# Performance work log

Hardware: AMD Instinct MI355X
Metric: run time of the kernel (lower is better)

## Reference

```python
import jax, jax.numpy as jnp
import numpy as np
from jax import lax

B, N, C = 8, 4096, 512
NH, R = 8, 8
HD = C // NH
EPS = 1e-3  # keras LayerNormalization default epsilon


def setup_inputs() -> dict:
    key = jax.random.key(0)
    ks = jax.random.split(key, 8)
    s = 0.02
    x = jax.random.normal(ks[0], (B, N, C), dtype=jnp.float32)
    Wq = jax.random.normal(ks[1], (C, C), dtype=jnp.float32) * s
    Wkv = jax.random.normal(ks[2], (C, 2 * C), dtype=jnp.float32) * s
    conv_w = jax.random.normal(ks[3], (R, R, C, C), dtype=jnp.float32) * s  # HWIO
    gamma = jnp.ones((C,), dtype=jnp.float32)
    beta = jnp.zeros((C,), dtype=jnp.float32)
    Wp = jax.random.normal(ks[4], (C, C), dtype=jnp.float32) * s
    bp = jnp.zeros((C,), dtype=jnp.float32)
    return {"x": x, "Wq": Wq, "Wkv": Wkv, "conv_w": conv_w,
            "gamma": gamma, "beta": beta, "Wp": Wp, "bp": bp}


def reference(x, Wq, Wkv, conv_w, gamma, beta, Wp, bp):
    b, n, c = x.shape
    h = w = int(np.sqrt(n))
    scale = 1.0 / np.sqrt(float(HD))

    # queries: Rearrange 'b n (hd nh) -> b n nh hd' then 'b n nh hd -> b nh n hd'
    q = x @ Wq                                   # [B, N, C]
    q = q.reshape(b, n, HD, NH).transpose(0, 3, 1, 2)  # [B, NH, N, HD]

    # spatial reduction of K/V: strided conv (SAME) + layernorm
    fmap = x.reshape(b, h, w, c)
    fmap = lax.conv_general_dilated(
        fmap, conv_w, window_strides=(R, R), padding="SAME",
        dimension_numbers=("NHWC", "HWIO", "NHWC"))   # [B, h/R, w/R, C]
    m = fmap.shape[1] * fmap.shape[2]
    fmap = fmap.reshape(b, m, c)
    mu = jnp.mean(fmap, axis=-1, keepdims=True)
    var = jnp.var(fmap, axis=-1, keepdims=True)
    fmap = (fmap - mu) * lax.rsqrt(var + EPS) * gamma + beta

    # key/value: Rearrange 'b m (f nh hd) -> b m f nh hd', perm [2,0,3,1,4]
    kv = fmap @ Wkv                              # [B, M, 2C]
    kv = kv.reshape(b, m, 2, NH, HD).transpose(2, 0, 3, 1, 4)  # [2, B, NH, M, HD]
    k, v = kv[0], kv[1]

    attn = jax.nn.softmax(jnp.einsum("bhnd,bhmd->bhnm", q, k) * scale, axis=-1)
    out = jnp.einsum("bhnm,bhmd->bhnd", attn, v)  # [B, NH, N, HD]
    out = out.transpose(0, 2, 1, 3).reshape(b, n, c)  # 'b n h c -> b n (h c)'
    return out @ Wp + bp
```

## Files before the change

### kernel.cpp

```cpp
#include <hip/hip_runtime.h>

typedef unsigned short u16;
typedef __bf16 bf16x8 __attribute__((ext_vector_type(8)));
typedef float floatx4 __attribute__((ext_vector_type(4)));

__device__ __forceinline__ u16 f2bf(float f) {
    unsigned u = __float_as_uint(f);
    u += 0x7fff + ((u >> 16) & 1);
    return (u16)(u >> 16);
}

#define GLOAD_LDS16(g, l) __builtin_amdgcn_global_load_lds( \
    (const __attribute__((address_space(1))) void*)(g),      \
    (__attribute__((address_space(3))) void*)(l), 16, 0, 0)

__global__ void cast_f32_bf16(const float* __restrict__ in, u16* __restrict__ out) {
    size_t o = ((size_t)blockIdx.x * 256 + threadIdx.x) * 4;
    float4 v = *(const float4*)(in + o);
    unsigned w0 = (unsigned)f2bf(v.x) | ((unsigned)f2bf(v.y) << 16);
    unsigned w1 = (unsigned)f2bf(v.z) | ((unsigned)f2bf(v.w) << 16);
    *(uint2*)(out + o) = make_uint2(w0, w1);
}

__global__ void transpose_cast(const float* __restrict__ in, u16* __restrict__ out,
                               int R, int Cn) {
    __shared__ float tile[32][33];
    int c0 = blockIdx.x * 32, r0 = blockIdx.y * 32;
    int tx = threadIdx.x, ty = threadIdx.y;
    #pragma unroll
    for (int yy = 0; yy < 4; ++yy)
        tile[ty + yy * 8][tx] = in[(size_t)(r0 + ty + yy * 8) * Cn + c0 + tx];
    __syncthreads();
    #pragma unroll
    for (int yy = 0; yy < 4; ++yy)
        out[(size_t)(c0 + ty + yy * 8) * R + r0 + tx] = f2bf(tile[tx][ty + yy * 8]);
}

__global__ void transpose_cast_qperm(const float* __restrict__ in, u16* __restrict__ out) {
    __shared__ float tile[32][33];
    int c0 = blockIdx.x * 32, r0 = blockIdx.y * 32;
    int tx = threadIdx.x, ty = threadIdx.y;
    #pragma unroll
    for (int yy = 0; yy < 4; ++yy)
        tile[ty + yy * 8][tx] = in[(size_t)(r0 + ty + yy * 8) * 512 + c0 + tx];
    __syncthreads();
    #pragma unroll
    for (int yy = 0; yy < 4; ++yy) {
        int cc = c0 + ty + yy * 8;
        int np = (cc & 7) * 64 + (cc >> 3);
        out[(size_t)np * 512 + r0 + tx] = f2bf(tile[tx][ty + yy * 8]);
    }
}

template<int MODE, int ASRC>
__global__ __launch_bounds__(256) void gemm_bt(
    const u16* __restrict__ A, const u16* __restrict__ B, float* __restrict__ out,
    int M, int N, int K, int KC, const float* __restrict__ bias)
{
    __shared__ u16 As[2][128 * 32];
    __shared__ u16 Bs[2][128 * 32];
    const int tid = threadIdx.x;
    const int wv = tid >> 6, lane = tid & 63;
    const int quad = lane >> 4, l15 = lane & 15;
    const int bm = blockIdx.y * 128, bn = blockIdx.x * 128;
    const int k0 = blockIdx.z * KC;
    const int wr = wv >> 1, wc = wv & 1;

    floatx4 acc[4][4];
    #pragma unroll
    for (int i = 0; i < 4; ++i)
        #pragma unroll
        for (int j = 0; j < 4; ++j)
            acc[i][j] = (floatx4){0.f, 0.f, 0.f, 0.f};

    for (int kt = 0; kt < KC; kt += 64) {
        const int kk = k0 + kt;
        #pragma unroll
        for (int hf = 0; hf < 2; ++hf) {
            #pragma unroll
            for (int c2 = 0; c2 < 2; ++c2) {
                int idx = ((wv * 2 + c2) * 64 + lane) * 8;
                int row = idx >> 5, col = idx & 31;
                int k = kk + hf * 32 + col;
                if (ASRC == 0) {
                    const u16* ga = A + (size_t)(bm + row) * K + k;
                    GLOAD_LDS16(ga, &As[hf][(wv * 2 + c2) * 512]);
                } else {
                    int p = bm + row;
                    int b = p >> 6, ij = p & 63, ii = ij >> 3, jj = ij & 7;
                    int r12 = k >> 9, r1 = r12 >> 3, r2 = r12 & 7;
                    int n = (ii * 8 + r1) * 64 + jj * 8 + r2;
                    const u16* ga = A + ((size_t)(b * 4096 + n)) * 512 + (k & 511);
                    GLOAD_LDS16(ga, &As[hf][(wv * 2 + c2) * 512]);
                }
                const u16* gb = B + (size_t)(bn + row) * K + k;
                GLOAD_LDS16(gb, &Bs[hf][(wv * 2 + c2) * 512]);
            }
        }
        __syncthreads();
        #pragma unroll
        for (int ks = 0; ks < 2; ++ks) {
            bf16x8 af[4], bfr[4];
            #pragma unroll
            for (int i = 0; i < 4; ++i)
                af[i] = *(const bf16x8*)&As[ks][(wr * 64 + i * 16 + l15) * 32 + quad * 8];
            #pragma unroll
            for (int j = 0; j < 4; ++j)
                bfr[j] = *(const bf16x8*)&Bs[ks][(wc * 64 + j * 16 + l15) * 32 + quad * 8];
            #pragma unroll
            for (int i = 0; i < 4; ++i)
                #pragma unroll
                for (int j = 0; j < 4; ++j)
                    acc[i][j] = __builtin_amdgcn_mfma_f32_16x16x32_bf16(af[i], bfr[j], acc[i][j], 0, 0, 0);
        }
        __syncthreads();
    }

    #pragma unroll
    for (int i = 0; i < 4; ++i) {
        #pragma unroll
        for (int j = 0; j < 4; ++j) {
            #pragma unroll
            for (int r = 0; r < 4; ++r) {
                int m = bm + wr * 64 + i * 16 + quad * 4 + r;
                int n = bn + wc * 64 + j * 16 + l15;
                float v = acc[i][j][r];
                if (MODE == 0) {
                    out[(size_t)blockIdx.z * 262144 + (size_t)m * N + n] = v;
                } else if (MODE == 1) {
                    int b = m >> 12, nn = m & 4095;
                    int h = n >> 6, d = n & 63;
                    ((u16*)out)[((size_t)((b * 8 + h) * 4096 + nn)) * 64 + d] = f2bf(v);
                } else if (MODE == 2) {
                    int b = m >> 6, mm = m & 63;
                    int f = n >> 9, c = n & 511, h = c >> 6, d = c & 63;
                    size_t idx;
                    if (f == 0) idx = ((size_t)((b * 8 + h) * 64 + mm)) * 64 + d;
                    else        idx = 262144 + ((size_t)((b * 8 + h) * 64 + d)) * 64 + mm;
                    atomicAdd(&out[idx], v);
                } else {
                    out[(size_t)m * 512 + n] = v + bias[n];
                }
            }
        }
    }
}

__global__ __launch_bounds__(256) void reduce_ln_bf16(
    const float* __restrict__ part, u16* __restrict__ out,
    const float* __restrict__ gamma, const float* __restrict__ beta)
{
    int row = blockIdx.x, tid = threadIdx.x;
    const float* base = part + (size_t)row * 512 + tid * 2;
    float2 v = {0.f, 0.f};
    #pragma unroll 8
    for (int z = 0; z < 64; ++z) {
        float2 t = *(const float2*)(base + (size_t)z * 262144);
        v.x += t.x; v.y += t.y;
    }
    float s = v.x + v.y, ss = v.x * v.x + v.y * v.y;
    #pragma unroll
    for (int off = 32; off > 0; off >>= 1) {
        s  += __shfl_down(s, off);
        ss += __shfl_down(ss, off);
    }
    __shared__ float red[8];
    __shared__ float stats[2];
    int wvi = tid >> 6, lane = tid & 63;
    if (lane == 0) { red[wvi * 2] = s; red[wvi * 2 + 1] = ss; }
    __syncthreads();
    if (tid == 0) {
        float S = red[0] + red[2] + red[4] + red[6];
        float SS = red[1] + red[3] + red[5] + red[7];
        float mean = S * (1.f / 512.f);
        float var = SS * (1.f / 512.f) - mean * mean;
        stats[0] = mean; stats[1] = rsqrtf(var + 1e-3f);
    }
    __syncthreads();
    float mean = stats[0], rstd = stats[1];
    float o0 = (v.x - mean) * rstd * gamma[tid * 2]     + beta[tid * 2];
    float o1 = (v.y - mean) * rstd * gamma[tid * 2 + 1] + beta[tid * 2 + 1];
    unsigned w = (unsigned)f2bf(o0) | ((unsigned)f2bf(o1) << 16);
    *(unsigned*)&out[(size_t)row * 512 + tid * 2] = w;
}

__global__ __launch_bounds__(256) void attn_mfma(
    const u16* __restrict__ qbf, const float* __restrict__ kvf, u16* __restrict__ attn_out)
{
    __shared__ u16 Ksh[64 * 64];
    __shared__ u16 Vt[64 * 64];
    __shared__ u16 Psh[4][32 * 64];
    const int bh = blockIdx.x, qt = blockIdx.y;
    const int tid = threadIdx.x;
    const int wv = tid >> 6, lane = tid & 63;
    const int quad = lane >> 4, l15 = lane & 15;

    {
        const float* kb = kvf + (size_t)bh * 4096;
        const float* vb = kvf + 262144 + (size_t)bh * 4096;
        for (int t = tid; t < 2048; t += 256) {
            float2 a = ((const float2*)kb)[t];
            ((unsigned*)Ksh)[t] = (unsigned)f2bf(a.x) | ((unsigned)f2bf(a.y) << 16);
            float2 b2 = ((const float2*)vb)[t];
            ((unsigned*)Vt)[t] = (unsigned)f2bf(b2.x) | ((unsigned)f2bf(b2.y) << 16);
        }
    }
    __syncthreads();

    const u16* qb = qbf + ((size_t)bh * 4096 + qt * 128 + wv * 32) * 64;
    bf16x8 qf[2][2];
    #pragma unroll
    for (int i = 0; i < 2; ++i)
        #pragma unroll
        for (int ks = 0; ks < 2; ++ks)
            qf[i][ks] = *(const bf16x8*)(qb + (i * 16 + l15) * 64 + ks * 32 + quad * 8);

    floatx4 s[2][4];
    #pragma unroll
    for (int i = 0; i < 2; ++i)
        #pragma unroll
        for (int j = 0; j < 4; ++j)
            s[i][j] = (floatx4){0.f, 0.f, 0.f, 0.f};
    #pragma unroll
    for (int j = 0; j < 4; ++j) {
        #pragma unroll
        for (int ks = 0; ks < 2; ++ks) {
            bf16x8 kf = *(const bf16x8*)&Ksh[(j * 16 + l15) * 64 + ks * 32 + quad * 8];
            #pragma unroll
            for (int i = 0; i < 2; ++i)
                s[i][j] = __builtin_amdgcn_mfma_f32_16x16x32_bf16(qf[i][ks], kf, s[i][j], 0, 0, 0);
        }
    }

    u16* P = Psh[wv];
    float rs[2][4];
    #pragma unroll
    for (int i = 0; i < 2; ++i)
        #pragma unroll
        for (int r = 0; r < 4; ++r) rs[i][r] = 0.f;
    #pragma unroll
    for (int i = 0; i < 2; ++i)
        #pragma unroll
        for (int j = 0; j < 4; ++j)
            #pragma unroll
            for (int r = 0; r < 4; ++r) {
                float e = __expf(s[i][j][r] * 0.125f);
                rs[i][r] += e;
                P[(i * 16 + quad * 4 + r) * 64 + j * 16 + l15] = f2bf(e);
            }
    #pragma unroll
    for (int m = 1; m < 16; m <<= 1)
        #pragma unroll
        for (int i = 0; i < 2; ++i)
            #pragma unroll
            for (int r = 0; r < 4; ++r)
                rs[i][r] += __shfl_xor(rs[i][r], m);
    __syncthreads();

    floatx4 o[2][4];
    #pragma unroll
    for (int i = 0; i < 2; ++i)
        #pragma unroll
        for (int j = 0; j < 4; ++j)
            o[i][j] = (floatx4){0.f, 0.f, 0.f, 0.f};
    #pragma unroll
    for (int ks = 0; ks < 2; ++ks) {
        bf16x8 pf[2];
        #pragma unroll
        for (int i = 0; i < 2; ++i)
            pf[i] = *(const bf16x8*)&P[(i * 16 + l15) * 64 + ks * 32 + quad * 8];
        #pragma unroll
        for (int j = 0; j < 4; ++j) {
            bf16x8 vf = *(const bf16x8*)&Vt[(j * 16 + l15) * 64 + ks * 32 + quad * 8];
            #pragma unroll
            for (int i = 0; i < 2; ++i)
                o[i][j] = __builtin_amdgcn_mfma_f32_16x16x32_bf16(pf[i], vf, o[i][j], 0, 0, 0);
        }
    }

    const int b = bh >> 3, h = bh & 7;
    #pragma unroll
    for (int i = 0; i < 2; ++i) {
        #pragma unroll
        for (int r = 0; r < 4; ++r) {
            float inv = 1.f / rs[i][r];
            int n = qt * 128 + wv * 32 + i * 16 + quad * 4 + r;
            u16* op = attn_out + ((size_t)(b * 4096 + n)) * 512 + h * 64;
            #pragma unroll
            for (int j = 0; j < 4; ++j)
                op[j * 16 + l15] = f2bf(o[i][j][r] * inv);
        }
    }
}

extern "C" void kernel_launch(void* const* d_in, const int* in_sizes, int n_in,
                              void* d_out, int out_size, void* d_ws, size_t ws_size,
                              hipStream_t stream) {
    const float* x      = (const float*)d_in[0];
    const float* Wq     = (const float*)d_in[1];
    const float* Wkv    = (const float*)d_in[2];
    const float* conv_w = (const float*)d_in[3];
    const float* gamma  = (const float*)d_in[4];
    const float* beta   = (const float*)d_in[5];
    const float* Wp     = (const float*)d_in[6];
    const float* bp     = (const float*)d_in[7];
    float* out = (float*)d_out;

    char* w = (char*)d_ws;
    const size_t MB = 1ull << 20;
    u16*   x_bf      = (u16*)(w + 0);
    u16*   WconvT    = (u16*)(w + 32 * MB);
    u16*   WqTp      = (u16*)(w + 64 * MB);
    u16*   WkvT      = (u16*)(w + 65 * MB);
    u16*   WpT       = (u16*)(w + 66 * MB);
    u16*   q_bf      = (u16*)(w + 67 * MB);
    float* fmap_part = (float*)(w + 99 * MB);
    u16*   fmap_ln   = (u16*)(w + 163 * MB);
    float* kv_f      = (float*)(w + 164 * MB);
    u16*   attn_bf   = (u16*)(w + 166 * MB);

    hipMemsetAsync(kv_f, 0, 2 * 262144 * 4, stream);

    cast_f32_bf16<<<16384, 256, 0, stream>>>(x, x_bf);
    transpose_cast_qperm<<<dim3(16, 16), dim3(32, 8), 0, stream>>>(Wq, WqTp);
    transpose_cast<<<dim3(32, 16),   dim3(32, 8), 0, stream>>>(Wkv,    WkvT,   512,   1024);
    transpose_cast<<<dim3(16, 1024), dim3(32, 8), 0, stream>>>(conv_w, WconvT, 32768, 512);
    transpose_cast<<<dim3(16, 16),   dim3(32, 8), 0, stream>>>(Wp,     WpT,    512,   512);

    gemm_bt<1, 0><<<dim3(4, 256, 1), 256, 0, stream>>>(x_bf, WqTp, (float*)q_bf, 32768, 512, 512, 512, nullptr);
    gemm_bt<0, 1><<<dim3(4, 4, 64), 256, 0, stream>>>(x_bf, WconvT, fmap_part, 512, 512, 32768, 512, nullptr);
    reduce_ln_bf16<<<512, 256, 0, stream>>>(fmap_part, fmap_ln, gamma, beta);
    gemm_bt<2, 0><<<dim3(8, 4, 4), 256, 0, stream>>>(fmap_ln, WkvT, kv_f, 512, 1024, 512, 128, nullptr);
    attn_mfma<<<dim3(64, 32), 256, 0, stream>>>(q_bf, kv_f, attn_bf);
    gemm_bt<3, 0><<<dim3(4, 256, 1), 256, 0, stream>>>(attn_bf, WpT, out, 32768, 512, 512, 512, bp);
}
```

Baseline: 360.7 us.

## Fuse prep kernels, store conv partials as bf16, drop KV split-K atomics

```diff
diff --git a/kernel.cpp b/kernel.cpp
--- a/kernel.cpp
+++ b/kernel.cpp
@@ -14,41 +14,41 @@
     (const __attribute__((address_space(1))) void*)(g),      \
     (__attribute__((address_space(3))) void*)(l), 16, 0, 0)
 
-__global__ void cast_f32_bf16(const float* __restrict__ in, u16* __restrict__ out) {
-    size_t o = ((size_t)blockIdx.x * 256 + threadIdx.x) * 4;
-    float4 v = *(const float4*)(in + o);
-    unsigned w0 = (unsigned)f2bf(v.x) | ((unsigned)f2bf(v.y) << 16);
-    unsigned w1 = (unsigned)f2bf(v.z) | ((unsigned)f2bf(v.w) << 16);
-    *(uint2*)(out + o) = make_uint2(w0, w1);
-}
-
-__global__ void transpose_cast(const float* __restrict__ in, u16* __restrict__ out,
-                               int R, int Cn) {
+__global__ __launch_bounds__(256) void prep_kernel(
+    const float* __restrict__ x, u16* __restrict__ x_bf,
+    const float* __restrict__ conv_w, u16* __restrict__ WconvT,
+    const float* __restrict__ Wq, u16* __restrict__ WqTp,
+    const float* __restrict__ Wp, u16* __restrict__ WpT,
+    const float* __restrict__ Wkv, u16* __restrict__ WkvT)
+{
+    int blk = blockIdx.x;
+    const int tid = threadIdx.x;
+    if (blk < 16384) {
+        size_t o = ((size_t)blk * 256 + tid) * 4;
+        float4 v = *(const float4*)(x + o);
+        unsigned w0 = (unsigned)f2bf(v.x) | ((unsigned)f2bf(v.y) << 16);
+        unsigned w1 = (unsigned)f2bf(v.z) | ((unsigned)f2bf(v.w) << 16);
+        *(uint2*)(x_bf + o) = make_uint2(w0, w1);
+        return;
+    }
+    blk -= 16384;
+    const float* in; u16* outp; int R, Cn, bx, by; bool perm = false;
+    if (blk < 16384)      { in = conv_w; outp = WconvT; R = 32768; Cn = 512;  bx = blk & 15; by = blk >> 4; }
+    else if (blk < 16640) { blk -= 16384; in = Wq;  outp = WqTp; R = 512; Cn = 512;  bx = blk & 15; by = blk >> 4; perm = true; }
+    else if (blk < 16896) { blk -= 16640; in = Wp;  outp = WpT;  R = 512; Cn = 512;  bx = blk & 15; by = blk >> 4; }
+    else                  { blk -= 16896; in = Wkv; outp = WkvT; R = 512; Cn = 1024; bx = blk & 31; by = blk >> 5; }
     __shared__ float tile[32][33];
-    int c0 = blockIdx.x * 32, r0 = blockIdx.y * 32;
-    int tx = threadIdx.x, ty = threadIdx.y;
+    const int c0 = bx * 32, r0 = by * 32;
+    const int tx = tid & 31, ty = tid >> 5;
     #pragma unroll
     for (int yy = 0; yy < 4; ++yy)
         tile[ty + yy * 8][tx] = in[(size_t)(r0 + ty + yy * 8) * Cn + c0 + tx];
     __syncthreads();
     #pragma unroll
-    for (int yy = 0; yy < 4; ++yy)
-        out[(size_t)(c0 + ty + yy * 8) * R + r0 + tx] = f2bf(tile[tx][ty + yy * 8]);
-}
-
-__global__ void transpose_cast_qperm(const float* __restrict__ in, u16* __restrict__ out) {
-    __shared__ float tile[32][33];
-    int c0 = blockIdx.x * 32, r0 = blockIdx.y * 32;
-    int tx = threadIdx.x, ty = threadIdx.y;
-    #pragma unroll
-    for (int yy = 0; yy < 4; ++yy)
-        tile[ty + yy * 8][tx] = in[(size_t)(r0 + ty + yy * 8) * 512 + c0 + tx];
-    __syncthreads();
-    #pragma unroll
     for (int yy = 0; yy < 4; ++yy) {
         int cc = c0 + ty + yy * 8;
-        int np = (cc & 7) * 64 + (cc >> 3);
-        out[(size_t)np * 512 + r0 + tx] = f2bf(tile[tx][ty + yy * 8]);
+        int np = perm ? ((cc & 7) * 64 + (cc >> 3)) : cc;
+        outp[(size_t)np * R + r0 + tx] = f2bf(tile[tx][ty + yy * 8]);
     }
 }
 
@@ -126,7 +126,7 @@
                 int n = bn + wc * 64 + j * 16 + l15;
                 float v = acc[i][j][r];
                 if (MODE == 0) {
-                    out[(size_t)blockIdx.z * 262144 + (size_t)m * N + n] = v;
+                    ((u16*)out)[(size_t)blockIdx.z * 262144 + (size_t)m * N + n] = f2bf(v);
                 } else if (MODE == 1) {
                     int b = m >> 12, nn = m & 4095;
                     int h = n >> 6, d = n & 63;
@@ -137,7 +137,7 @@
                     size_t idx;
                     if (f == 0) idx = ((size_t)((b * 8 + h) * 64 + mm)) * 64 + d;
                     else        idx = 262144 + ((size_t)((b * 8 + h) * 64 + d)) * 64 + mm;
-                    atomicAdd(&out[idx], v);
+                    out[idx] = v;
                 } else {
                     out[(size_t)m * 512 + n] = v + bias[n];
                 }
@@ -147,16 +147,17 @@
 }
 
 __global__ __launch_bounds__(256) void reduce_ln_bf16(
-    const float* __restrict__ part, u16* __restrict__ out,
+    const u16* __restrict__ part, u16* __restrict__ out,
     const float* __restrict__ gamma, const float* __restrict__ beta)
 {
     int row = blockIdx.x, tid = threadIdx.x;
-    const float* base = part + (size_t)row * 512 + tid * 2;
+    const unsigned* base = (const unsigned*)(part + (size_t)row * 512) + tid;
     float2 v = {0.f, 0.f};
     #pragma unroll 8
     for (int z = 0; z < 64; ++z) {
-        float2 t = *(const float2*)(base + (size_t)z * 262144);
-        v.x += t.x; v.y += t.y;
+        unsigned u = base[(size_t)z * 131072];
+        v.x += __uint_as_float(u << 16);
+        v.y += __uint_as_float(u & 0xffff0000u);
     }
     float s = v.x + v.y, ss = v.x * v.x + v.y * v.y;
     #pragma unroll
@@ -314,23 +315,17 @@
     u16*   WkvT      = (u16*)(w + 65 * MB);
     u16*   WpT       = (u16*)(w + 66 * MB);
     u16*   q_bf      = (u16*)(w + 67 * MB);
-    float* fmap_part = (float*)(w + 99 * MB);
-    u16*   fmap_ln   = (u16*)(w + 163 * MB);
-    float* kv_f      = (float*)(w + 164 * MB);
-    u16*   attn_bf   = (u16*)(w + 166 * MB);
-
-    hipMemsetAsync(kv_f, 0, 2 * 262144 * 4, stream);
-
-    cast_f32_bf16<<<16384, 256, 0, stream>>>(x, x_bf);
-    transpose_cast_qperm<<<dim3(16, 16), dim3(32, 8), 0, stream>>>(Wq, WqTp);
-    transpose_cast<<<dim3(32, 16),   dim3(32, 8), 0, stream>>>(Wkv,    WkvT,   512,   1024);
-    transpose_cast<<<dim3(16, 1024), dim3(32, 8), 0, stream>>>(conv_w, WconvT, 32768, 512);
-    transpose_cast<<<dim3(16, 16),   dim3(32, 8), 0, stream>>>(Wp,     WpT,    512,   512);
+    u16*   fmap_part = (u16*)(w + 99 * MB);
+    u16*   fmap_ln   = (u16*)(w + 131 * MB);
+    float* kv_f      = (float*)(w + 132 * MB);
+    u16*   attn_bf   = (u16*)(w + 134 * MB);
+
+    prep_kernel<<<33792, 256, 0, stream>>>(x, x_bf, conv_w, WconvT, Wq, WqTp, Wp, WpT, Wkv, WkvT);
 
     gemm_bt<1, 0><<<dim3(4, 256, 1), 256, 0, stream>>>(x_bf, WqTp, (float*)q_bf, 32768, 512, 512, 512, nullptr);
-    gemm_bt<0, 1><<<dim3(4, 4, 64), 256, 0, stream>>>(x_bf, WconvT, fmap_part, 512, 512, 32768, 512, nullptr);
+    gemm_bt<0, 1><<<dim3(4, 4, 64), 256, 0, stream>>>(x_bf, WconvT, (float*)fmap_part, 512, 512, 32768, 512, nullptr);
     reduce_ln_bf16<<<512, 256, 0, stream>>>(fmap_part, fmap_ln, gamma, beta);
-    gemm_bt<2, 0><<<dim3(8, 4, 4), 256, 0, stream>>>(fmap_ln, WkvT, kv_f, 512, 1024, 512, 128, nullptr);
+    gemm_bt<2, 0><<<dim3(8, 4, 1), 256, 0, stream>>>(fmap_ln, WkvT, kv_f, 512, 1024, 512, 512, nullptr);
     attn_mfma<<<dim3(64, 32), 256, 0, stream>>>(q_bf, kv_f, attn_bf);
     gemm_bt<3, 0><<<dim3(4, 256, 1), 256, 0, stream>>>(attn_bf, WpT, out, 32768, 512, 512, 512, bp);
 }
```

After: 335.3 us. 1.08x faster.
